# Kernel optimization log

Hardware: AMD Instinct MI355X
Metric: run time of the kernel (lower is better)

## Reference

```python
import jax, jax.numpy as jnp
import numpy as np

D_MODEL = 768; D_KV = 64; H = 12; D_FF = 3072; L = 2
TP = 4; SP = 16; MT = 16; MS = 4
MASK_RATE = 0.2; EPS = 1e-6
B = 256; T = 64; F = 64
ST = (T // TP) * (F // SP)  # 64 tokens


def ln(x, s, b):
    mu = jnp.mean(x, -1, keepdims=True)
    var = jnp.mean(jnp.square(x - mu), -1, keepdims=True)
    return (x - mu) * jax.lax.rsqrt(var + EPS) * s + b


def mha(x, Wq, bq, Wk, bk, Wv, bv, Wo, bo):
    Bz, S, D = x.shape
    q = (x @ Wq + bq).reshape(Bz, S, H, D_KV)
    k = (x @ Wk + bk).reshape(Bz, S, H, D_KV)
    v = (x @ Wv + bv).reshape(Bz, S, H, D_KV)
    scores = jnp.einsum('bqhd,bkhd->bhqk', q, k) * (D_KV ** -0.5)
    attn = jax.nn.softmax(scores, axis=-1)
    o = jnp.einsum('bhqk,bkhd->bqhd', attn, v).reshape(Bz, S, H * D_KV)
    return o @ Wo + bo


def setup_inputs():
    key = jax.random.key(0)
    ks = jax.random.split(key, 16)
    s = 0.02
    nrm = lambda k, shp: jax.random.normal(k, shp, jnp.float32) * s
    return {
        'inputs': jax.random.normal(ks[0], (B, T, F, 1), jnp.float32),
        'randomness': jax.random.uniform(ks[1], (B * ST, 3), jnp.float32),
        'perm': jax.random.permutation(ks[2], B * ST),
        'conv_w': nrm(ks[3], (TP, SP, 1, D_MODEL)), 'conv_b': jnp.zeros((D_MODEL,)),
        'temp_embd': nrm(ks[4], (MT, D_MODEL)), 'spec_embd': nrm(ks[5], (MS, D_MODEL)),
        'pos_ln_s': jnp.ones((D_MODEL,)), 'pos_ln_b': jnp.zeros((D_MODEL,)),
        'mask_tok': nrm(ks[6], (D_MODEL,)), 'agg_tok': nrm(ks[7], (D_MODEL,)),
        'Wq': nrm(ks[8], (L, D_MODEL, H * D_KV)), 'bq': jnp.zeros((L, H * D_KV)),
        'Wk': nrm(ks[9], (L, D_MODEL, H * D_KV)), 'bk': jnp.zeros((L, H * D_KV)),
        'Wv': nrm(ks[10], (L, D_MODEL, H * D_KV)), 'bv': jnp.zeros((L, H * D_KV)),
        'Wo': nrm(ks[11], (L, H * D_KV, D_MODEL)), 'bo': jnp.zeros((L, D_MODEL)),
        'ln1_s': jnp.ones((L, D_MODEL)), 'ln1_b': jnp.zeros((L, D_MODEL)),
        'W1': nrm(ks[12], (L, D_MODEL, D_FF)), 'b1': jnp.zeros((L, D_FF)),
        'W2': nrm(ks[13], (L, D_FF, D_MODEL)), 'b2': jnp.zeros((L, D_MODEL)),
        'ln2_s': jnp.ones((L, D_MODEL)), 'ln2_b': jnp.zeros((L, D_MODEL)),
    }


def reference(inputs, randomness, perm, conv_w, conv_b, temp_embd, spec_embd,
              pos_ln_s, pos_ln_b, mask_tok, agg_tok, Wq, bq, Wk, bk, Wv, bv,
              Wo, bo, ln1_s, ln1_b, W1, b1, W2, b2, ln2_s, ln2_b):
    # Conv2D patchify: [B, T, F, 1] -> [B, T/4, F/16, d_model]
    x = jax.lax.conv_general_dilated(
        inputs, conv_w, (TP, SP), 'VALID',
        dimension_numbers=('NHWC', 'HWIO', 'NHWC')) + conv_b
    Bz, Tt, Ss, D = x.shape
    e = x.reshape(Bz, Tt * Ss, D)  # token embeddings [B, 64, 768]
    # Vectorized BERT-style random masking (replaces the per-element sparse-scatter loop)
    sel = randomness[:, 0] <= MASK_RATE
    m = (sel & (randomness[:, 1] <= 0.8)).astype(e.dtype).reshape(Bz, Tt * Ss)
    rnd = (sel & (randomness[:, 1] > 0.8) & (randomness[:, 2] <= 0.5)).astype(e.dtype).reshape(Bz, Tt * Ss)
    shuffled = jax.lax.stop_gradient(e.reshape(-1, D))[perm].reshape(Bz, Tt * Ss, D)
    me = e * (1.0 - m - rnd)[..., None] + mask_tok * m[..., None] + shuffled * rnd[..., None]
    # Spectro-temporal position embeddings + LN
    pos = (temp_embd[:Tt, None, :] + spec_embd[None, :Ss, :]).reshape(Tt * Ss, D)
    h = ln(me + pos, pos_ln_s, pos_ln_b)
    # Prepend AGG token
    h = jnp.concatenate([jnp.broadcast_to(agg_tok, (Bz, 1, D)), h], axis=1)
    # Post-norm transformer encoder
    for l in range(L):
        a = mha(h, Wq[l], bq[l], Wk[l], bk[l], Wv[l], bv[l], Wo[l], bo[l])
        h = ln(h + a, ln1_s[l], ln1_b[l])
        f = jax.nn.gelu(h @ W1[l] + b1[l], approximate=False) @ W2[l] + b2[l]
        h = ln(h + f, ln2_s[l], ln2_b[l])
    return h  # last_hidden_states [B, 65, 768]; aggregated=h[:,0], predictions=h[:,1:]
```

## Files before the change

kernel.cpp:

```cpp
#include <hip/hip_runtime.h>
#include <hip/hip_bf16.h>
#include <math.h>

using bf16 = __hip_bfloat16;
typedef __bf16 bf16x8v __attribute__((ext_vector_type(8)));
typedef float f32x4 __attribute__((ext_vector_type(4)));
typedef unsigned short ushort4v __attribute__((ext_vector_type(4)));
typedef unsigned short ushort8v __attribute__((ext_vector_type(8)));

__device__ __forceinline__ float b2f(bf16 x) { return __bfloat162float(x); }
__device__ __forceinline__ bf16 f2b(float x) { return __float2bfloat16(x); }

__device__ __forceinline__ void gload_lds16(const void* g, void* l) {
  __builtin_amdgcn_global_load_lds(
      (__attribute__((address_space(1))) void*)(void*)g,
      (__attribute__((address_space(3))) void*)l, 16, 0, 0);
}

__device__ __forceinline__ float block_sum(float v, float* buf) {
  #pragma unroll
  for (int off = 32; off > 0; off >>= 1) v += __shfl_xor(v, off);
  __syncthreads();
  if ((threadIdx.x & 63) == 0) buf[threadIdx.x >> 6] = v;
  __syncthreads();
  return buf[0] + buf[1] + buf[2] + buf[3];
}

__global__ __launch_bounds__(256) void transpose_kernel(
    const float* __restrict__ in, bf16* __restrict__ out, int K, int N) {
  __shared__ float tile[32][33];
  const int nbx = N >> 5;
  const int bx = blockIdx.x % nbx, by = blockIdx.x / nbx;
  const int tx = threadIdx.x & 31, ty = threadIdx.x >> 5;
  #pragma unroll
  for (int i = 0; i < 4; ++i) {
    const int r = by * 32 + ty + i * 8;
    tile[ty + i * 8][tx] = in[(size_t)r * N + bx * 32 + tx];
  }
  __syncthreads();
  #pragma unroll
  for (int i = 0; i < 4; ++i) {
    const int r = bx * 32 + ty + i * 8;
    out[(size_t)r * K + by * 32 + tx] = f2b(tile[tx][ty + i * 8]);
  }
}

__global__ __launch_bounds__(256) void biasqkv_kernel(
    const float* __restrict__ bq, const float* __restrict__ bk,
    const float* __restrict__ bv, float* __restrict__ out) {
  const int i = blockIdx.x * 256 + threadIdx.x;
  if (i >= 2 * 2304) return;
  const int l = i / 2304, n = i % 2304;
  float v = (n < 768) ? bq[l * 768 + n]
          : (n < 1536) ? bk[l * 768 + n - 768] : bv[l * 768 + n - 1536];
  out[i] = v;
}

__global__ __launch_bounds__(256) void patchify_kernel(
    const float* __restrict__ in, const float* __restrict__ w,
    const float* __restrict__ cb, bf16* __restrict__ e) {
  __shared__ float patch[8][64];
  const int tid = threadIdx.x;
  const int tok0 = blockIdx.x * 8;
  for (int idx = tid; idx < 512; idx += 256) {
    const int t = idx >> 6, p = idx & 63;
    const int tok = tok0 + t;
    const int b = tok >> 6, t2 = tok & 63, tt = t2 >> 2, ss = t2 & 3;
    const int kt = p >> 4, kf = p & 15;
    patch[t][p] = in[((size_t)b * 64 + tt * 4 + kt) * 64 + ss * 16 + kf];
  }
  __syncthreads();
  for (int i = 0; i < 3; ++i) {
    const int d = tid + i * 256;
    const float cbv = cb[d];
    float acc[8];
    #pragma unroll
    for (int t = 0; t < 8; ++t) acc[t] = cbv;
    for (int p = 0; p < 64; ++p) {
      const float wv = w[p * 768 + d];
      #pragma unroll
      for (int t = 0; t < 8; ++t) acc[t] += patch[t][p] * wv;
    }
    #pragma unroll
    for (int t = 0; t < 8; ++t) e[(size_t)(tok0 + t) * 768 + d] = f2b(acc[t]);
  }
}

__global__ __launch_bounds__(256) void embed_kernel(
    const bf16* __restrict__ e, const float* __restrict__ randomness,
    const int* __restrict__ perm, const float* __restrict__ temp_embd,
    const float* __restrict__ spec_embd, const float* __restrict__ pls,
    const float* __restrict__ plb, const float* __restrict__ mask_tok,
    const float* __restrict__ agg_tok, bf16* __restrict__ h) {
  __shared__ float rbuf[4];
  const int row = blockIdx.x;
  const int b = row / 65, s = row % 65;
  const int tid = threadIdx.x;
  const size_t ob = (size_t)row * 768;
  if (s == 0) {
    #pragma unroll
    for (int i = 0; i < 3; ++i) { const int d = tid + i * 256; h[ob + d] = f2b(agg_tok[d]); }
    return;
  }
  const int tok = s - 1;
  const int gt = b * 64 + tok;
  const float r0 = randomness[gt * 3 + 0];
  const float r1 = randomness[gt * 3 + 1];
  const float r2 = randomness[gt * 3 + 2];
  const bool selb = (r0 <= 0.2f);
  const bool mflag = selb && (r1 <= 0.8f);
  const bool rflag = selb && (r1 > 0.8f) && (r2 <= 0.5f);
  const int src = rflag ? perm[gt] : gt;
  const int tt = tok >> 2, ss2 = tok & 3;
  float v[3]; float sum = 0.f;
  #pragma unroll
  for (int i = 0; i < 3; ++i) {
    const int d = tid + i * 256;
    const float ev = mflag ? mask_tok[d] : b2f(e[(size_t)src * 768 + d]);
    v[i] = ev + temp_embd[tt * 768 + d] + spec_embd[ss2 * 768 + d];
    sum += v[i];
  }
  const float mu = block_sum(sum, rbuf) * (1.f / 768.f);
  float q = 0.f;
  #pragma unroll
  for (int i = 0; i < 3; ++i) { const float t = v[i] - mu; q += t * t; }
  const float rstd = rsqrtf(block_sum(q, rbuf) * (1.f / 768.f) + 1e-6f);
  #pragma unroll
  for (int i = 0; i < 3; ++i) {
    const int d = tid + i * 256;
    h[ob + d] = f2b((v[i] - mu) * rstd * pls[d] + plb[d]);
  }
}

template <int F32OUT>
__global__ __launch_bounds__(256) void resln_kernel(
    const bf16* __restrict__ x, const bf16* __restrict__ y,
    const float* __restrict__ sc, const float* __restrict__ bi,
    void* __restrict__ outp) {
  __shared__ float rbuf[4];
  const int tid = threadIdx.x;
  const size_t base = (size_t)blockIdx.x * 768;
  float v[3]; float s = 0.f;
  #pragma unroll
  for (int i = 0; i < 3; ++i) {
    const int d = tid + i * 256;
    v[i] = b2f(x[base + d]) + b2f(y[base + d]);
    s += v[i];
  }
  const float mu = block_sum(s, rbuf) * (1.f / 768.f);
  float q = 0.f;
  #pragma unroll
  for (int i = 0; i < 3; ++i) { const float t = v[i] - mu; q += t * t; }
  const float rstd = rsqrtf(block_sum(q, rbuf) * (1.f / 768.f) + 1e-6f);
  #pragma unroll
  for (int i = 0; i < 3; ++i) {
    const int d = tid + i * 256;
    const float o = (v[i] - mu) * rstd * sc[d] + bi[d];
    if (F32OUT) ((float*)outp)[base + d] = o;
    else        ((bf16*)outp)[base + d] = f2b(o);
  }
}

template <int WN, int ACT>
__global__ __launch_bounds__(512, 2) void gemm256_kernel(
    const unsigned short* __restrict__ A, const unsigned short* __restrict__ BT,
    const float* __restrict__ bias, bf16* __restrict__ C, int N, int K, int nbn) {
  constexpr int WM = 8 / WN;
  constexpr int RPW = 256 / WM;
  constexpr int BN = 64 * WN;
  constexpr int MF = RPW / 16;
  constexpr int NF = 4;
  constexpr int ABYTES = 256 * 128;
  constexpr int BBYTES = BN * 128;
  constexpr int PADC = BN + 4;
  constexpr int LOOPB = 2 * (ABYTES + BBYTES);
  constexpr int EPIB = 256 * PADC * 2;
  constexpr int SMEMB = LOOPB > EPIB ? LOOPB : EPIB;
  __shared__ __align__(16) char smem[SMEMB];

  const int nwg = gridDim.x;
  const int orig = blockIdx.x;
  const int q8 = nwg >> 3, r8 = nwg & 7;
  const int xcd = orig & 7, lin = orig >> 3;
  const int bid = (xcd < r8 ? xcd * (q8 + 1) : r8 * (q8 + 1) + (xcd - r8) * q8) + lin;
  const int bm = bid / nbn, bn = bid % nbn;

  const int tid = threadIdx.x;
  const int w = tid >> 6, lane = tid & 63;
  const int wrow = w / WN, wcol = w % WN;
  const int frow = lane & 15;
  const int kgrp = lane & 48;

  const size_t Kb = (size_t)K * 2;
  const int laneRow = lane >> 3;
  const int laneCB = ((lane & 7) << 4) ^ (lane & 32);
  const char* gA = (const char*)A + ((size_t)bm * 256 + w * 8 + laneRow) * Kb + laneCB;
  const char* gB = (const char*)BT + ((size_t)bn * BN + w * 8 + laneRow) * Kb + laneCB;

  f32x4 acc[MF][NF];
  #pragma unroll
  for (int i = 0; i < MF; ++i)
    #pragma unroll
    for (int j = 0; j < NF; ++j) acc[i][j] = f32x4{0.f, 0.f, 0.f, 0.f};

  auto stage = [&](int buf, int kt) {
    const size_t ko = (size_t)kt << 7;
    char* la = smem + buf * (ABYTES + BBYTES);
    char* lb = la + ABYTES;
    #pragma unroll
    for (int i = 0; i < 4; ++i)
      gload_lds16(gA + (size_t)i * 64 * Kb + ko, la + i * 8192 + w * 1024);
    #pragma unroll
    for (int i = 0; i < BN / 64; ++i)
      gload_lds16(gB + (size_t)i * 64 * Kb + ko, lb + i * 8192 + w * 1024);
  };

  auto compute = [&](int buf) {
    const char* la = smem + buf * (ABYTES + BBYTES);
    const char* lb = la + ABYTES;
    #pragma unroll
    for (int mq = 0; mq < MF / 4; ++mq) {
      bf16x8v af[4][2];
      #pragma unroll
      for (int j = 0; j < 4; ++j)
        #pragma unroll
        for (int s = 0; s < 2; ++s) {
          const int row = wrow * RPW + (mq * 4 + j) * 16 + frow;
          const int cb = (s * 64 + kgrp) ^ (((row >> 2) & 1) << 5);
          af[j][s] = *(const bf16x8v*)(la + row * 128 + cb);
        }
      #pragma unroll
      for (int nq = 0; nq < 2; ++nq) {
        bf16x8v bv[2][2];
        #pragma unroll
        for (int n = 0; n < 2; ++n)
          #pragma unroll
          for (int s = 0; s < 2; ++s) {
            const int row = wcol * 64 + (nq * 2 + n) * 16 + frow;
            const int cb = (s * 64 + kgrp) ^ (((row >> 2) & 1) << 5);
            bv[n][s] = *(const bf16x8v*)(lb + row * 128 + cb);
          }
        #pragma unroll
        for (int j = 0; j < 4; ++j)
          #pragma unroll
          for (int n = 0; n < 2; ++n) {
            acc[mq * 4 + j][nq * 2 + n] = __builtin_amdgcn_mfma_f32_16x16x32_bf16(
                af[j][0], bv[n][0], acc[mq * 4 + j][nq * 2 + n], 0, 0, 0);
            acc[mq * 4 + j][nq * 2 + n] = __builtin_amdgcn_mfma_f32_16x16x32_bf16(
                af[j][1], bv[n][1], acc[mq * 4 + j][nq * 2 + n], 0, 0, 0);
          }
      }
    }
  };

  const int NT = K >> 6;
  stage(0, 0);
  __syncthreads();
  int cur = 0;
  for (int t = 0; t < NT; ++t) {
    if (t + 1 < NT) stage(cur ^ 1, t + 1);
    compute(cur);
    __syncthreads();
    cur ^= 1;
  }

  bf16* cb16 = (bf16*)smem;
  #pragma unroll
  for (int mf = 0; mf < MF; ++mf)
    #pragma unroll
    for (int nf = 0; nf < NF; ++nf) {
      const int col = wcol * 64 + nf * 16 + frow;
      const float bvv = bias[bn * BN + col];
      #pragma unroll
      for (int r = 0; r < 4; ++r) {
        const int row = wrow * RPW + mf * 16 + ((lane >> 4) << 2) + r;
        float v = acc[mf][nf][r] + bvv;
        if (ACT == 1) v = 0.5f * v * (1.0f + erff(v * 0.70710678f));
        cb16[row * PADC + col] = f2b(v);
      }
    }
  __syncthreads();
  constexpr int CPR = BN / 8;
  #pragma unroll
  for (int j = 0; j < 256 * CPR / 512; ++j) {
    const int idx = tid + j * 512;
    const int row = idx / CPR, c = idx % CPR;
    const ushort8v val = *(const ushort8v*)(cb16 + row * PADC + c * 8);
    *(ushort8v*)(C + ((size_t)bm * 256 + row) * N + bn * BN + c * 8) = val;
  }
}

__global__ __launch_bounds__(320) void attn_mfma_kernel(
    const bf16* __restrict__ qkv, bf16* __restrict__ ctx) {
  __shared__ __align__(16) bf16 sK[80][72];
  __shared__ __align__(16) bf16 sVt[64][104];
  __shared__ __align__(16) bf16 sP[5][16][104];
  const int b = blockIdx.x / 12, h = blockIdx.x % 12;
  const int tid = threadIdx.x;
  const int wave = tid >> 6, lane = tid & 63;
  const size_t base = ((size_t)b * 65) * 2304 + (size_t)h * 64;
  const bf16 bzero = f2b(0.f);

  for (int idx = tid; idx < 65 * 16; idx += 320) {
    const int row = idx >> 4, d4 = (idx & 15) * 4;
    const ushort4v kv = *(const ushort4v*)(qkv + base + (size_t)row * 2304 + 768 + d4);
    const ushort4v vv = *(const ushort4v*)(qkv + base + (size_t)row * 2304 + 1536 + d4);
    *(ushort4v*)&sK[row][d4] = kv;
    #pragma unroll
    for (int j = 0; j < 4; ++j) ((unsigned short*)&sVt[d4 + j][row])[0] = vv[j];
  }
  for (int idx = tid; idx < 15 * 16; idx += 320) {
    const int row = 65 + (idx >> 4), d4 = (idx & 15) * 4;
    *(ushort4v*)&sK[row][d4] = ushort4v{0, 0, 0, 0};
  }
  for (int idx = tid; idx < 64 * 31; idx += 320) {
    const int d = idx / 31, c = 65 + (idx % 31);
    sVt[d][c] = bzero;
  }
  __syncthreads();

  const int frow = lane & 15;
  const int koff = (lane >> 4) * 8;
  const int row0 = wave * 16;
  const int qrow = (row0 + frow > 64) ? 64 : (row0 + frow);
  const bf16* qptr = qkv + base + (size_t)qrow * 2304;
  const bf16x8v aq0 = *(const bf16x8v*)(qptr + koff);
  const bf16x8v aq1 = *(const bf16x8v*)(qptr + 32 + koff);

  const f32x4 z4 = {0.f, 0.f, 0.f, 0.f};
  f32x4 sacc[5];
  #pragma unroll
  for (int n = 0; n < 5; ++n) sacc[n] = z4;
  #pragma unroll
  for (int n = 0; n < 5; ++n) {
    const bf16x8v b0 = *(const bf16x8v*)&sK[n * 16 + frow][koff];
    const bf16x8v b1 = *(const bf16x8v*)&sK[n * 16 + frow][32 + koff];
    sacc[n] = __builtin_amdgcn_mfma_f32_16x16x32_bf16(aq0, b0, sacc[n], 0, 0, 0);
    sacc[n] = __builtin_amdgcn_mfma_f32_16x16x32_bf16(aq1, b1, sacc[n], 0, 0, 0);
  }

  #pragma unroll
  for (int r = 0; r < 4; ++r) {
    const int prow = ((lane >> 4) << 2) + r;
    float v[5];
    float mx = -1e30f;
    #pragma unroll
    for (int n = 0; n < 5; ++n) {
      const int col = n * 16 + frow;
      v[n] = (col < 65) ? sacc[n][r] * 0.125f : -1e30f;
      mx = fmaxf(mx, v[n]);
    }
    #pragma unroll
    for (int off = 1; off < 16; off <<= 1) mx = fmaxf(mx, __shfl_xor(mx, off));
    float sum = 0.f;
    #pragma unroll
    for (int n = 0; n < 5; ++n) { v[n] = __expf(v[n] - mx); sum += v[n]; }
    #pragma unroll
    for (int off = 1; off < 16; off <<= 1) sum += __shfl_xor(sum, off);
    const float inv = 1.f / sum;
    #pragma unroll
    for (int n = 0; n < 5; ++n)
      sP[wave][prow][n * 16 + frow] = f2b(v[n] * inv);
    sP[wave][prow][80 + frow] = bzero;
  }

  f32x4 oacc[4];
  #pragma unroll
  for (int n = 0; n < 4; ++n) oacc[n] = z4;
  #pragma unroll
  for (int kk = 0; kk < 3; ++kk) {
    const bf16x8v ap = *(const bf16x8v*)&sP[wave][frow][kk * 32 + koff];
    #pragma unroll
    for (int n = 0; n < 4; ++n) {
      const bf16x8v bv = *(const bf16x8v*)&sVt[n * 16 + frow][kk * 32 + koff];
      oacc[n] = __builtin_amdgcn_mfma_f32_16x16x32_bf16(ap, bv, oacc[n], 0, 0, 0);
    }
  }

  #pragma unroll
  for (int r = 0; r < 4; ++r) {
    const int row = row0 + ((lane >> 4) << 2) + r;
    if (row < 65) {
      bf16* op = ctx + ((size_t)b * 65 + row) * 768 + (size_t)h * 64 + frow;
      #pragma unroll
      for (int n = 0; n < 4; ++n) op[n * 16] = f2b(oacc[n][r]);
    }
  }
}

extern "C" void kernel_launch(void* const* d_in, const int* in_sizes, int n_in,
                              void* d_out, int out_size, void* d_ws, size_t ws_size,
                              hipStream_t stream) {
  (void)in_sizes; (void)n_in; (void)out_size; (void)ws_size;
  const float* inputs     = (const float*)d_in[0];
  const float* randomness = (const float*)d_in[1];
  const int*   perm       = (const int*)d_in[2];
  const float* conv_w     = (const float*)d_in[3];
  const float* conv_b     = (const float*)d_in[4];
  const float* temp_embd  = (const float*)d_in[5];
  const float* spec_embd  = (const float*)d_in[6];
  const float* pos_ln_s   = (const float*)d_in[7];
  const float* pos_ln_b   = (const float*)d_in[8];
  const float* mask_tok   = (const float*)d_in[9];
  const float* agg_tok    = (const float*)d_in[10];
  const float* Wq = (const float*)d_in[11]; const float* bq = (const float*)d_in[12];
  const float* Wk = (const float*)d_in[13]; const float* bk = (const float*)d_in[14];
  const float* Wv = (const float*)d_in[15]; const float* bv = (const float*)d_in[16];
  const float* Wo = (const float*)d_in[17]; const float* bo = (const float*)d_in[18];
  const float* ln1_s = (const float*)d_in[19]; const float* ln1_b = (const float*)d_in[20];
  const float* W1 = (const float*)d_in[21]; const float* b1 = (const float*)d_in[22];
  const float* W2 = (const float*)d_in[23]; const float* b2 = (const float*)d_in[24];
  const float* ln2_s = (const float*)d_in[25]; const float* ln2_b = (const float*)d_in[26];

  char* wsb = (char*)d_ws;
  size_t off = 0;
  auto carve = [&](size_t bytes) { char* p = wsb + off; off = (off + bytes + 255) & ~(size_t)255; return p; };
  bf16* wqkvT = (bf16*)carve((size_t)2 * 2304 * 768 * 2);
  bf16* woT   = (bf16*)carve((size_t)2 * 768 * 768 * 2);
  bf16* w1T   = (bf16*)carve((size_t)2 * 3072 * 768 * 2);
  bf16* w2T   = (bf16*)carve((size_t)2 * 768 * 3072 * 2);
  float* bqkv = (float*)carve((size_t)2 * 2304 * 4);
  bf16* ebuf  = (bf16*)carve((size_t)16640 * 768 * 2);
  bf16* hbuf  = (bf16*)carve((size_t)16640 * 768 * 2);
  bf16* qkvb  = (bf16*)carve((size_t)16640 * 2304 * 2);
  bf16* ctxb  = (bf16*)carve((size_t)16640 * 768 * 2);
  bf16* tmpb  = ebuf;
  bf16* midb  = qkvb;

  const dim3 blk(256);
  for (int l = 0; l < 2; ++l) {
    transpose_kernel<<<576, blk, 0, stream>>>(Wq + (size_t)l * 768 * 768, wqkvT + (size_t)l * 2304 * 768, 768, 768);
    transpose_kernel<<<576, blk, 0, stream>>>(Wk + (size_t)l * 768 * 768, wqkvT + (size_t)l * 2304 * 768 + 768 * 768, 768, 768);
    transpose_kernel<<<576, blk, 0, stream>>>(Wv + (size_t)l * 768 * 768, wqkvT + (size_t)l * 2304 * 768 + 2 * 768 * 768, 768, 768);
    transpose_kernel<<<576, blk, 0, stream>>>(Wo + (size_t)l * 768 * 768, woT + (size_t)l * 768 * 768, 768, 768);
    transpose_kernel<<<2304, blk, 0, stream>>>(W1 + (size_t)l * 768 * 3072, w1T + (size_t)l * 3072 * 768, 768, 3072);
    transpose_kernel<<<2304, blk, 0, stream>>>(W2 + (size_t)l * 3072 * 768, w2T + (size_t)l * 768 * 3072, 3072, 768);
  }
  biasqkv_kernel<<<18, blk, 0, stream>>>(bq, bk, bv, bqkv);
  patchify_kernel<<<2048, blk, 0, stream>>>(inputs, conv_w, conv_b, ebuf);
  embed_kernel<<<16640, blk, 0, stream>>>(ebuf, randomness, perm, temp_embd, spec_embd,
                                          pos_ln_s, pos_ln_b, mask_tok, agg_tok, hbuf);
  for (int l = 0; l < 2; ++l) {
    gemm256_kernel<4, 0><<<65 * 9, dim3(512), 0, stream>>>(
        (const unsigned short*)hbuf, (const unsigned short*)(wqkvT + (size_t)l * 2304 * 768),
        bqkv + l * 2304, qkvb, 2304, 768, 9);
    attn_mfma_kernel<<<256 * 12, dim3(320), 0, stream>>>(qkvb, ctxb);
    gemm256_kernel<2, 0><<<65 * 6, dim3(512), 0, stream>>>(
        (const unsigned short*)ctxb, (const unsigned short*)(woT + (size_t)l * 768 * 768),
        bo + l * 768, tmpb, 768, 768, 6);
    resln_kernel<0><<<16640, blk, 0, stream>>>(hbuf, tmpb, ln1_s + l * 768, ln1_b + l * 768, hbuf);
    gemm256_kernel<4, 1><<<65 * 12, dim3(512), 0, stream>>>(
        (const unsigned short*)hbuf, (const unsigned short*)(w1T + (size_t)l * 3072 * 768),
        b1 + l * 3072, midb, 3072, 768, 12);
    gemm256_kernel<2, 0><<<65 * 6, dim3(512), 0, stream>>>(
        (const unsigned short*)midb, (const unsigned short*)(w2T + (size_t)l * 768 * 3072),
        b2 + l * 768, tmpb, 768, 3072, 6);
    if (l == 1)
      resln_kernel<1><<<16640, blk, 0, stream>>>(hbuf, tmpb, ln2_s + l * 768, ln2_b + l * 768, d_out);
    else
      resln_kernel<0><<<16640, blk, 0, stream>>>(hbuf, tmpb, ln2_s + l * 768, ln2_b + l * 768, hbuf);
  }
}
```

Baseline: 966.9 us.

## Rewrite GEMM as fixed 256x256 tile with 8-phase barrier-interleaved MFMA pipeline

```diff
diff --git a/kernel.cpp b/kernel.cpp
--- a/kernel.cpp
+++ b/kernel.cpp
@@ -161,22 +161,11 @@
   }
 }
 
-template <int WN, int ACT>
-__global__ __launch_bounds__(512, 2) void gemm256_kernel(
+template <int ACT>
+__global__ __launch_bounds__(512, 2) void gemm8p_kernel(
     const unsigned short* __restrict__ A, const unsigned short* __restrict__ BT,
     const float* __restrict__ bias, bf16* __restrict__ C, int N, int K, int nbn) {
-  constexpr int WM = 8 / WN;
-  constexpr int RPW = 256 / WM;
-  constexpr int BN = 64 * WN;
-  constexpr int MF = RPW / 16;
-  constexpr int NF = 4;
-  constexpr int ABYTES = 256 * 128;
-  constexpr int BBYTES = BN * 128;
-  constexpr int PADC = BN + 4;
-  constexpr int LOOPB = 2 * (ABYTES + BBYTES);
-  constexpr int EPIB = 256 * PADC * 2;
-  constexpr int SMEMB = LOOPB > EPIB ? LOOPB : EPIB;
-  __shared__ __align__(16) char smem[SMEMB];
+  __shared__ __align__(16) char smem[131072];
 
   const int nwg = gridDim.x;
   const int orig = blockIdx.x;
@@ -187,106 +176,132 @@
 
   const int tid = threadIdx.x;
   const int w = tid >> 6, lane = tid & 63;
-  const int wrow = w / WN, wcol = w % WN;
+  const int wrow = w >> 2, wcol = w & 3;
   const int frow = lane & 15;
   const int kgrp = lane & 48;
+  const int rsw = (frow & 7) << 4;
+  const int cb0 = kgrp ^ rsw;
 
   const size_t Kb = (size_t)K * 2;
   const int laneRow = lane >> 3;
-  const int laneCB = ((lane & 7) << 4) ^ (lane & 32);
-  const char* gA = (const char*)A + ((size_t)bm * 256 + w * 8 + laneRow) * Kb + laneCB;
-  const char* gB = (const char*)BT + ((size_t)bn * BN + w * 8 + laneRow) * Kb + laneCB;
-
-  f32x4 acc[MF][NF];
-  #pragma unroll
-  for (int i = 0; i < MF; ++i)
-    #pragma unroll
-    for (int j = 0; j < NF; ++j) acc[i][j] = f32x4{0.f, 0.f, 0.f, 0.f};
-
-  auto stage = [&](int buf, int kt) {
+  const int srcCB = (((lane & 7) ^ laneRow) << 4);
+  const char* gA = (const char*)A + ((size_t)bm * 256 + w * 8 + laneRow) * Kb + srcCB;
+  const char* gB = (const char*)BT + ((size_t)bn * 256 + w * 8 + laneRow) * Kb + srcCB;
+
+  f32x4 acc[8][4];
+  #pragma unroll
+  for (int i = 0; i < 8; ++i)
+    #pragma unroll
+    for (int j = 0; j < 4; ++j) acc[i][j] = f32x4{0.f, 0.f, 0.f, 0.f};
+
+  auto issueTile = [&](int kt, int slot) {
+    char* la = smem + slot * 65536;
+    char* lb = la + 32768;
     const size_t ko = (size_t)kt << 7;
-    char* la = smem + buf * (ABYTES + BBYTES);
-    char* lb = la + ABYTES;
     #pragma unroll
     for (int i = 0; i < 4; ++i)
       gload_lds16(gA + (size_t)i * 64 * Kb + ko, la + i * 8192 + w * 1024);
     #pragma unroll
-    for (int i = 0; i < BN / 64; ++i)
+    for (int i = 0; i < 4; ++i)
       gload_lds16(gB + (size_t)i * 64 * Kb + ko, lb + i * 8192 + w * 1024);
   };
 
-  auto compute = [&](int buf) {
-    const char* la = smem + buf * (ABYTES + BBYTES);
-    const char* lb = la + ABYTES;
-    #pragma unroll
-    for (int mq = 0; mq < MF / 4; ++mq) {
-      bf16x8v af[4][2];
+  const int T = K >> 6;
+  issueTile(0, 0);
+
+  for (int t = 0; t < T; ++t) {
+    const int s = t & 1;
+    const char* la = smem + s * 65536;
+    const char* lb = la + 32768;
+
+    if (t + 1 < T) {
+      issueTile(t + 1, s ^ 1);
+      asm volatile("s_waitcnt vmcnt(8)" ::: "memory");
+    } else {
+      asm volatile("s_waitcnt vmcnt(0)" ::: "memory");
+    }
+    __builtin_amdgcn_s_barrier();
+    bf16x8v bfr[4][2], af[2][2];
+    #pragma unroll
+    for (int n = 0; n < 4; ++n) {
+      const int rB = (wcol * 64 + n * 16 + frow) * 128;
+      bfr[n][0] = *(const bf16x8v*)(lb + rB + cb0);
+      bfr[n][1] = *(const bf16x8v*)(lb + rB + (cb0 ^ 64));
+    }
+    {
+      const int rA = (wrow * 128 + frow) * 128;
+      af[0][0] = *(const bf16x8v*)(la + rA + cb0);
+      af[0][1] = *(const bf16x8v*)(la + rA + (cb0 ^ 64));
+      af[1][0] = *(const bf16x8v*)(la + rA + 2048 + cb0);
+      af[1][1] = *(const bf16x8v*)(la + rA + 2048 + (cb0 ^ 64));
+    }
+    asm volatile("s_waitcnt lgkmcnt(0)" ::: "memory");
+    __builtin_amdgcn_sched_barrier(0);
+    __builtin_amdgcn_s_setprio(1);
+    #pragma unroll
+    for (int j = 0; j < 2; ++j)
       #pragma unroll
-      for (int j = 0; j < 4; ++j)
+      for (int n = 0; n < 4; ++n) {
+        acc[j][n] = __builtin_amdgcn_mfma_f32_16x16x32_bf16(af[j][0], bfr[n][0], acc[j][n], 0, 0, 0);
+        acc[j][n] = __builtin_amdgcn_mfma_f32_16x16x32_bf16(af[j][1], bfr[n][1], acc[j][n], 0, 0, 0);
+      }
+    __builtin_amdgcn_s_setprio(0);
+    __builtin_amdgcn_s_barrier();
+
+    #pragma unroll
+    for (int p = 1; p < 4; ++p) {
+      const int rA = (wrow * 128 + p * 32 + frow) * 128;
+      af[0][0] = *(const bf16x8v*)(la + rA + cb0);
+      af[0][1] = *(const bf16x8v*)(la + rA + (cb0 ^ 64));
+      af[1][0] = *(const bf16x8v*)(la + rA + 2048 + cb0);
+      af[1][1] = *(const bf16x8v*)(la + rA + 2048 + (cb0 ^ 64));
+      __builtin_amdgcn_sched_barrier(0);
+      __builtin_amdgcn_s_barrier();
+      asm volatile("s_waitcnt lgkmcnt(0)" ::: "memory");
+      __builtin_amdgcn_sched_barrier(0);
+      __builtin_amdgcn_s_setprio(1);
+      #pragma unroll
+      for (int j = 0; j < 2; ++j)
         #pragma unroll
-        for (int s = 0; s < 2; ++s) {
-          const int row = wrow * RPW + (mq * 4 + j) * 16 + frow;
-          const int cb = (s * 64 + kgrp) ^ (((row >> 2) & 1) << 5);
-          af[j][s] = *(const bf16x8v*)(la + row * 128 + cb);
+        for (int n = 0; n < 4; ++n) {
+          acc[2 * p + j][n] = __builtin_amdgcn_mfma_f32_16x16x32_bf16(af[j][0], bfr[n][0], acc[2 * p + j][n], 0, 0, 0);
+          acc[2 * p + j][n] = __builtin_amdgcn_mfma_f32_16x16x32_bf16(af[j][1], bfr[n][1], acc[2 * p + j][n], 0, 0, 0);
         }
+      __builtin_amdgcn_s_setprio(0);
+      __builtin_amdgcn_s_barrier();
+    }
+  }
+
+  bf16* cbuf = (bf16*)smem;
+  float bias4[4];
+  #pragma unroll
+  for (int n = 0; n < 4; ++n) bias4[n] = bias[bn * 256 + wcol * 64 + n * 16 + frow];
+  const int rgrp = (lane >> 4) << 2;
+  #pragma unroll
+  for (int half = 0; half < 2; ++half) {
+    if (wrow == half) {
       #pragma unroll
-      for (int nq = 0; nq < 2; ++nq) {
-        bf16x8v bv[2][2];
+      for (int mf = 0; mf < 8; ++mf)
         #pragma unroll
-        for (int n = 0; n < 2; ++n)
+        for (int n = 0; n < 4; ++n) {
+          const int col = wcol * 64 + n * 16 + frow;
           #pragma unroll
-          for (int s = 0; s < 2; ++s) {
-            const int row = wcol * 64 + (nq * 2 + n) * 16 + frow;
-            const int cb = (s * 64 + kgrp) ^ (((row >> 2) & 1) << 5);
-            bv[n][s] = *(const bf16x8v*)(lb + row * 128 + cb);
+          for (int r = 0; r < 4; ++r) {
+            float v = acc[mf][n][r] + bias4[n];
+            if (ACT == 1) v = 0.5f * v * (1.0f + erff(v * 0.70710678f));
+            cbuf[(mf * 16 + rgrp + r) * 264 + col] = f2b(v);
           }
-        #pragma unroll
-        for (int j = 0; j < 4; ++j)
-          #pragma unroll
-          for (int n = 0; n < 2; ++n) {
-            acc[mq * 4 + j][nq * 2 + n] = __builtin_amdgcn_mfma_f32_16x16x32_bf16(
-                af[j][0], bv[n][0], acc[mq * 4 + j][nq * 2 + n], 0, 0, 0);
-            acc[mq * 4 + j][nq * 2 + n] = __builtin_amdgcn_mfma_f32_16x16x32_bf16(
-                af[j][1], bv[n][1], acc[mq * 4 + j][nq * 2 + n], 0, 0, 0);
-          }
-      }
-    }
-  };
-
-  const int NT = K >> 6;
-  stage(0, 0);
-  __syncthreads();
-  int cur = 0;
-  for (int t = 0; t < NT; ++t) {
-    if (t + 1 < NT) stage(cur ^ 1, t + 1);
-    compute(cur);
+        }
+    }
     __syncthreads();
-    cur ^= 1;
-  }
-
-  bf16* cb16 = (bf16*)smem;
-  #pragma unroll
-  for (int mf = 0; mf < MF; ++mf)
-    #pragma unroll
-    for (int nf = 0; nf < NF; ++nf) {
-      const int col = wcol * 64 + nf * 16 + frow;
-      const float bvv = bias[bn * BN + col];
-      #pragma unroll
-      for (int r = 0; r < 4; ++r) {
-        const int row = wrow * RPW + mf * 16 + ((lane >> 4) << 2) + r;
-        float v = acc[mf][nf][r] + bvv;
-        if (ACT == 1) v = 0.5f * v * (1.0f + erff(v * 0.70710678f));
-        cb16[row * PADC + col] = f2b(v);
-      }
-    }
-  __syncthreads();
-  constexpr int CPR = BN / 8;
-  #pragma unroll
-  for (int j = 0; j < 256 * CPR / 512; ++j) {
-    const int idx = tid + j * 512;
-    const int row = idx / CPR, c = idx % CPR;
-    const ushort8v val = *(const ushort8v*)(cb16 + row * PADC + c * 8);
-    *(ushort8v*)(C + ((size_t)bm * 256 + row) * N + bn * BN + c * 8) = val;
+    #pragma unroll
+    for (int jj = 0; jj < 8; ++jj) {
+      const int idx = tid + jj * 512;
+      const int rowl = idx >> 5, c = idx & 31;
+      const ushort8v val = *(const ushort8v*)(cbuf + rowl * 264 + c * 8);
+      *(ushort8v*)(C + ((size_t)(bm * 256 + half * 128 + rowl)) * N + (size_t)bn * 256 + c * 8) = val;
+    }
+    __syncthreads();
   }
 }
 
@@ -441,20 +456,20 @@
   embed_kernel<<<16640, blk, 0, stream>>>(ebuf, randomness, perm, temp_embd, spec_embd,
                                           pos_ln_s, pos_ln_b, mask_tok, agg_tok, hbuf);
   for (int l = 0; l < 2; ++l) {
-    gemm256_kernel<4, 0><<<65 * 9, dim3(512), 0, stream>>>(
+    gemm8p_kernel<0><<<65 * 9, dim3(512), 0, stream>>>(
         (const unsigned short*)hbuf, (const unsigned short*)(wqkvT + (size_t)l * 2304 * 768),
         bqkv + l * 2304, qkvb, 2304, 768, 9);
     attn_mfma_kernel<<<256 * 12, dim3(320), 0, stream>>>(qkvb, ctxb);
-    gemm256_kernel<2, 0><<<65 * 6, dim3(512), 0, stream>>>(
+    gemm8p_kernel<0><<<65 * 3, dim3(512), 0, stream>>>(
         (const unsigned short*)ctxb, (const unsigned short*)(woT + (size_t)l * 768 * 768),
-        bo + l * 768, tmpb, 768, 768, 6);
+        bo + l * 768, tmpb, 768, 768, 3);
     resln_kernel<0><<<16640, blk, 0, stream>>>(hbuf, tmpb, ln1_s + l * 768, ln1_b + l * 768, hbuf);
-    gemm256_kernel<4, 1><<<65 * 12, dim3(512), 0, stream>>>(
+    gemm8p_kernel<1><<<65 * 12, dim3(512), 0, stream>>>(
         (const unsigned short*)hbuf, (const unsigned short*)(w1T + (size_t)l * 3072 * 768),
         b1 + l * 3072, midb, 3072, 768, 12);
-    gemm256_kernel<2, 0><<<65 * 6, dim3(512), 0, stream>>>(
+    gemm8p_kernel<0><<<65 * 3, dim3(512), 0, stream>>>(
         (const unsigned short*)midb, (const unsigned short*)(w2T + (size_t)l * 768 * 3072),
-        b2 + l * 768, tmpb, 768, 3072, 6);
+        b2 + l * 768, tmpb, 768, 3072, 3);
     if (l == 1)
       resln_kernel<1><<<16640, blk, 0, stream>>>(hbuf, tmpb, ln2_s + l * 768, ln2_b + l * 768, d_out);
     else
```

New measurement: 1.065 ms. +10.2%, slower.
